# Kernel tuning notes

Measured on AMD Instinct MI355X. Metric: run time of the kernel, lower is better.

## Reference

```python
import jax, jax.numpy as jnp
import numpy as np

MAX_ABS = 1.0          # assumed get_max_abs('T')
DT = 0.01              # forward default dt
TWO_PI = 2.0 * np.pi
B, D, N = 4096, 2048, 4096


def setup_inputs() -> dict:
    key = jax.random.key(0)
    k0, k1 = jax.random.split(key, 2)
    x = jax.random.normal(k0, (B, D), dtype=jnp.float32)
    # nn.Linear params
    W = jax.random.normal(k1, (N, D), dtype=jnp.float32) * (1.0 / np.sqrt(D))
    b = jnp.zeros((N,), dtype=jnp.float32)
    # oscillator params (as initialized in __init__)
    amplitude = jnp.ones((N,), dtype=jnp.float32)
    frequency = jnp.ones((N,), dtype=jnp.float32)
    phase_offset = jnp.zeros((N,), dtype=jnp.float32)
    damping = jnp.full((N,), 0.01, dtype=jnp.float32)
    return {"x": x, "W": W, "b": b, "amplitude": amplitude,
            "frequency": frequency, "phase_offset": phase_offset,
            "damping": damping}


def reference(x, W, b, amplitude, frequency, phase_offset, damping):
    # driving force: [B, N]
    force = x @ W.T + b
    omega_sq = (TWO_PI * frequency) ** 2  # [N]
    # t starts at 0 and is incremented ONCE per forward call
    t = DT

    def step(carry, f):
        state, vel = carry
        accel = -omega_sq * state - damping * vel + f
        vel = vel + accel * DT
        state = state + vel * DT
        return (state, vel), state

    init = (jnp.zeros((N,), x.dtype), jnp.zeros((N,), x.dtype))
    (_, _), states = jax.lax.scan(step, init, force)  # states: [B, N]

    # sinusoid term is identical for every batch step (t fixed within forward)
    osc = amplitude * jnp.sin(TWO_PI * frequency * t + phase_offset)  # [N]
    out = jnp.clip(states + osc, -MAX_ABS, MAX_ABS)
    return out
```

## Files before the change

kernel.cpp:

```cpp
#include <hip/hip_runtime.h>
#include <hip/hip_bf16.h>
#include <math.h>

#define MDIM 4096
#define KDIM 2048
#define NDIM 4096
#define DT   0.01f
#define TWO_PI_F 6.283185307179586f
#define CH 64
#define CL 64
#define TILES (KDIM / 64)

typedef __attribute__((ext_vector_type(8))) short bf16x8;
typedef __attribute__((ext_vector_type(4))) float f32x4;

__device__ __forceinline__ unsigned short f2bf(float f) {
  unsigned int u = __float_as_uint(f);
  u += 0x7FFFu + ((u >> 16) & 1u);
  return (unsigned short)(u >> 16);
}
__device__ __forceinline__ float bf2f(unsigned short u) {
  return __uint_as_float(((unsigned int)u) << 16);
}

__global__ void cast2_bf16_kernel(const float* __restrict__ s0,
                                  unsigned short* __restrict__ d0,
                                  const float* __restrict__ s1,
                                  unsigned short* __restrict__ d1,
                                  int n4each) {
  int i = blockIdx.x * blockDim.x + threadIdx.x;
  const float4* sp;
  ushort4* dp;
  int j;
  if (i < n4each) { sp = (const float4*)s0; dp = (ushort4*)d0; j = i; }
  else            { sp = (const float4*)s1; dp = (ushort4*)d1; j = i - n4each; }
  float4 v = sp[j];
  ushort4 o;
  o.x = f2bf(v.x); o.y = f2bf(v.y); o.z = f2bf(v.z); o.w = f2bf(v.w);
  dp[j] = o;
}


__device__ __forceinline__ void gload16(const unsigned short* g,
                                        unsigned short* l) {
  __builtin_amdgcn_global_load_lds(
      (const __attribute__((address_space(1))) unsigned int*)g,
      (__attribute__((address_space(3))) unsigned int*)l, 16, 0, 0);
}

#define WAITVM(n) asm volatile("s_waitcnt vmcnt(" #n ")" ::: "memory")
#define WAITLGKM(n) asm volatile("s_waitcnt lgkmcnt(" #n ")" ::: "memory")
#define SCHEDB() __builtin_amdgcn_sched_barrier(0)

__global__ __launch_bounds__(512, 2) void gemm_scan256_kernel(
    const unsigned short* __restrict__ A,
    const unsigned short* __restrict__ Bm,
    const float* __restrict__ bias,
    const float* __restrict__ freq,
    const float* __restrict__ damp,
    unsigned short* __restrict__ zpart,
    float* __restrict__ chunkS,
    float* __restrict__ chunkV) {
  extern __shared__ __align__(16) unsigned short smem[];

  const int tid  = threadIdx.x;
  const int lane = tid & 63;
  const int w    = tid >> 6;
  const int wr   = w >> 2;
  const int wc   = w & 3;
  const int q    = lane >> 4;
  const int lm   = lane & 15;

  const int bid = blockIdx.x;
  const int wg  = (bid & 7) * 32 + (bid >> 3);
  const int tm  = wg >> 4;
  const int tn  = wg & 15;
  const int bM  = tm * 256;
  const int bN  = tn * 256;

  const int srow  = w * 16 + (lane >> 2);
  const int sslot = (lane & 3) ^ ((lane >> 3) & 3);
  const unsigned short* gA = A  + (size_t)(bM + srow) * KDIM + sslot * 8;
  const unsigned short* gB = Bm + (size_t)(bN + srow) * KDIM + sslot * 8;
  const int ldst = w * 512 + lane * 8;

#define SUNIT(mat, u, ks, rh)                                              \
  gload16((mat ? gB : gA) + (size_t)(rh) * 128 * KDIM + (u) * 64 + (ks) * 32, \
          smem + ((u) & 1) * 32768 + (mat) * 16384 + (ks) * 8192 +         \
              (rh) * 4096 + ldst)

  const int flane = (lm >> 1) & 3;
  const int aoff  = (wr * 128 + lm) * 32 + ((q ^ flane) * 8);
  const int boff  = 16384 + (wc * 64 + lm) * 32 + ((q ^ flane) * 8);

  f32x4 acc[8][4];
#pragma unroll
  for (int i = 0; i < 8; i++)
#pragma unroll
    for (int j = 0; j < 4; j++) acc[i][j] = (f32x4){0.f, 0.f, 0.f, 0.f};

  SUNIT(1, 0, 0, 0); SUNIT(1, 0, 0, 1);
  SUNIT(0, 0, 0, 0); SUNIT(0, 0, 0, 1);
  SUNIT(1, 0, 1, 0); SUNIT(1, 0, 1, 1);
  SUNIT(0, 0, 1, 0); SUNIT(0, 0, 1, 1);
  SUNIT(1, 1, 0, 0); SUNIT(1, 1, 0, 1);
  SUNIT(0, 1, 0, 0); SUNIT(0, 1, 0, 1);
  SUNIT(1, 1, 1, 0); SUNIT(1, 1, 1, 1);

#define LDA4(dst, BUFO, KS, MH)                                            \
  _Pragma("unroll") for (int m = 0; m < 4; ++m) dst[m] =                   \
      *(const bf16x8*)&smem[(BUFO) + (KS) + (MH) + aoff + m * 512]
#define LDB4(dst, BUFO, KS)                                                \
  _Pragma("unroll") for (int n = 0; n < 4; ++n) dst[n] =                   \
      *(const bf16x8*)&smem[(BUFO) + (KS) + boff + n * 512]
#define MFMA16(AF, BF, MB)                                                 \
  __builtin_amdgcn_s_setprio(1);                                          \
  _Pragma("unroll") for (int m = 0; m < 4; ++m)                            \
      _Pragma("unroll") for (int n = 0; n < 4; ++n)                        \
          acc[(MB) + m][n] = __builtin_amdgcn_mfma_f32_16x16x32_bf16(      \
              AF[m], BF[n], acc[(MB) + m][n], 0, 0, 0);                    \
  __builtin_amdgcn_s_setprio(0)

  bf16x8 af[4], bfr[4];

  WAITVM(10);
  __builtin_amdgcn_s_barrier();
  LDA4(af, 0, 0, 0);
  LDB4(bfr, 0, 0);
  SCHEDB();

#pragma unroll 2
  for (int t = 0; t < TILES; ++t) {
    const int bufo  = (t & 1) * 32768;
    const int nbufo = ((t + 1) & 1) * 32768;

    __builtin_amdgcn_s_barrier();
    if (t + 1 < TILES) { SUNIT(0, t + 1, 1, 0); SUNIT(0, t + 1, 1, 1); }
    WAITLGKM(0); SCHEDB();
    MFMA16(af, bfr, 0);
    LDA4(af, bufo, 0, 2048);
    SCHEDB();

    if (t < TILES - 1) { WAITVM(8); } else { WAITVM(0); }
    __builtin_amdgcn_s_barrier();
    if (t + 2 < TILES) { SUNIT(1, t + 2, 0, 0); SUNIT(1, t + 2, 0, 1); }
    WAITLGKM(0); SCHEDB();
    MFMA16(af, bfr, 4);
    LDA4(af, bufo, 8192, 0);
    LDB4(bfr, bufo, 8192);
    SCHEDB();

    __builtin_amdgcn_s_barrier();
    if (t + 2 < TILES) { SUNIT(0, t + 2, 0, 0); SUNIT(0, t + 2, 0, 1); }
    WAITLGKM(0); SCHEDB();
    MFMA16(af, bfr, 0);
    LDA4(af, bufo, 8192, 2048);
    SCHEDB();

    if (t < TILES - 2) { WAITVM(8); }
    else if (t == TILES - 2) { WAITVM(4); }
    __builtin_amdgcn_s_barrier();
    if (t + 2 < TILES) { SUNIT(1, t + 2, 1, 0); SUNIT(1, t + 2, 1, 1); }
    WAITLGKM(0); SCHEDB();
    MFMA16(af, bfr, 4);
    if (t + 1 < TILES) {
      LDA4(af, nbufo, 0, 0);
      LDB4(bfr, nbufo, 0);
      SCHEDB();
    }
  }
#undef LDA4
#undef LDB4
#undef MFMA16
#undef SUNIT

  __syncthreads();

#pragma unroll
  for (int n = 0; n < 4; ++n) {
    const float bz = bias[bN + wc * 64 + n * 16 + lm];
#pragma unroll
    for (int M = 0; M < 8; ++M)
#pragma unroll
      for (int rr = 0; rr < 4; ++rr) {
        const int row = wr * 128 + M * 16 + q * 4 + rr;
        const int col = wc * 64 + ((n ^ q) * 16) + lm;
        smem[row * 256 + col] = f2bf(acc[M][n][rr] + bz);
      }
  }
  __syncthreads();

  {
    const int col  = tid & 255;
    const int ch0  = (tid >> 8) * 2;
    const int gcol = bN + col;
    const float om  = TWO_PI_F * freq[gcol];
    const float osq = om * om;
    const float dp  = damp[gcol];
#pragma unroll
    for (int cc = 0; cc < 2; ++cc) {
      const int ch = ch0 + cc;
      float s = 0.f, v = 0.f;
#pragma unroll 8
      for (int i = 0; i < CL; ++i) {
        const int row = ch * 64 + i;
        const int idx = row * 256 + (col ^ (((i >> 2) & 3) << 4));
        float f = bf2f(smem[idx]);
        v += (-osq * s - dp * v + f) * DT;
        s += v * DT;
        smem[idx] = f2bf(s);
      }
      const int chunk = tm * 4 + ch;
      chunkS[chunk * NDIM + gcol] = s;
      chunkV[chunk * NDIM + gcol] = v;
    }
  }
  __syncthreads();

#pragma unroll
  for (int k = 0; k < 16; ++k) {
    const int slot = tid + 512 * k;
    const int row  = slot >> 5;
    const int grp  = slot & 31;
    const int sgrp = grp ^ (((row >> 2) & 3) << 1);
    *(uint4*)&zpart[(size_t)(bM + row) * NDIM + bN + grp * 8] =
        *(const uint4*)&smem[row * 256 + sgrp * 8];
  }
}

__global__ void scan_pass2_inplace(float* __restrict__ chunkS,
                                   float* __restrict__ chunkV,
                                   const float* __restrict__ freq,
                                   const float* __restrict__ damp) {
  int n = blockIdx.x * blockDim.x + threadIdx.x;
  float om = TWO_PI_F * freq[n];
  float osq = om * om;
  float dp = damp[n];
  float a00 = 1.f - osq * DT * DT, a01 = DT * (1.f - dp * DT);
  float a10 = -osq * DT,           a11 = 1.f - dp * DT;
#pragma unroll
  for (int i = 0; i < 6; i++) {
    float b00 = a00 * a00 + a01 * a10;
    float b01 = a00 * a01 + a01 * a11;
    float b10 = a10 * a00 + a11 * a10;
    float b11 = a10 * a01 + a11 * a11;
    a00 = b00; a01 = b01; a10 = b10; a11 = b11;
  }
  float cs = 0.f, cv = 0.f;
#pragma unroll 8
  for (int c = 0; c < CH; c++) {
    float ls = chunkS[c * NDIM + n];
    float lv = chunkV[c * NDIM + n];
    chunkS[c * NDIM + n] = cs;
    chunkV[c * NDIM + n] = cv;
    float ns = a00 * cs + a01 * cv + ls;
    float nv = a10 * cs + a11 * cv + lv;
    cs = ns; cv = nv;
  }
}

__global__ void scan_out_carry4(const unsigned short* __restrict__ zpart,
                                const float* __restrict__ amp,
                                const float* __restrict__ freq,
                                const float* __restrict__ phase,
                                const float* __restrict__ damp,
                                const float* __restrict__ carryS,
                                const float* __restrict__ carryV,
                                float* __restrict__ out) {
  int gid = blockIdx.x * blockDim.x + threadIdx.x;
  int n4 = gid & (NDIM / 4 - 1);
  int cq = gid >> 10;
  int c  = cq >> 2;
  int qq = cq & 3;
  int n  = n4 * 4;

  float4 fr = *(const float4*)&freq[n];
  float4 dv = *(const float4*)&damp[n];
  float4 am = *(const float4*)&amp[n];
  float4 ph = *(const float4*)&phase[n];
  float omv[4] = {TWO_PI_F * fr.x, TWO_PI_F * fr.y, TWO_PI_F * fr.z, TWO_PI_F * fr.w};
  float dpv[4] = {dv.x, dv.y, dv.z, dv.w};
  float amv[4] = {am.x, am.y, am.z, am.w};
  float phv[4] = {ph.x, ph.y, ph.z, ph.w};
  float m00[4], m01[4], m10[4], m11[4], osc[4];
#pragma unroll
  for (int j = 0; j < 4; j++) {
    float osq = omv[j] * omv[j];
    m00[j] = 1.f - osq * DT * DT;  m01[j] = DT * (1.f - dpv[j] * DT);
    m10[j] = -osq * DT;            m11[j] = 1.f - dpv[j] * DT;
    osc[j] = amv[j] * sinf(omv[j] * DT + phv[j]);
  }

  float4 csv = *(const float4*)&carryS[c * NDIM + n];
  float4 cvv = *(const float4*)&carryV[c * NDIM + n];
  float cs[4] = {csv.x, csv.y, csv.z, csv.w};
  float cv[4] = {cvv.x, cvv.y, cvv.z, cvv.w};
  float hs[4], hv[4];
#pragma unroll
  for (int j = 0; j < 4; j++) {
    float p00 = m00[j], p01 = m01[j], p10 = m10[j], p11 = m11[j];
#pragma unroll
    for (int k = 0; k < 4; k++) {
      float b00 = p00 * p00 + p01 * p10;
      float b01 = p00 * p01 + p01 * p11;
      float b10 = p10 * p00 + p11 * p10;
      float b11 = p10 * p01 + p11 * p11;
      p00 = b00; p01 = b01; p10 = b10; p11 = b11;
    }
    float j00 = 1.f, j01 = 0.f, j10 = 0.f, j11 = 1.f;
    for (int k = 0; k < qq; k++) {
      float b00 = j00 * p00 + j01 * p10;
      float b01 = j00 * p01 + j01 * p11;
      float b10 = j10 * p00 + j11 * p10;
      float b11 = j10 * p01 + j11 * p11;
      j00 = b00; j01 = b01; j10 = b10; j11 = b11;
    }
    hs[j] = j00 * cs[j] + j01 * cv[j];
    hv[j] = j10 * cs[j] + j11 * cv[j];
  }

  const size_t r0 = (size_t)c * CL + qq * 16;
  const unsigned short* zp = zpart + r0 * NDIM + n;
  float* op = out + r0 * NDIM + n;
#pragma unroll 4
  for (int i = 0; i < 16; ++i) {
    ushort4 zv = *(const ushort4*)&zp[(size_t)i * NDIM];
    float z[4] = {bf2f(zv.x), bf2f(zv.y), bf2f(zv.z), bf2f(zv.w)};
    float o[4];
#pragma unroll
    for (int j = 0; j < 4; j++) {
      float t = m00[j] * hs[j] + m01[j] * hv[j];
      float u = m10[j] * hs[j] + m11[j] * hv[j];
      hs[j] = t; hv[j] = u;
      o[j] = fminf(1.f, fmaxf(-1.f, hs[j] + z[j] + osc[j]));
    }
    *(float4*)&op[(size_t)i * NDIM] = (float4){o[0], o[1], o[2], o[3]};
  }
}

__global__ __launch_bounds__(256, 2) void gemm_bt_kernel(
    const unsigned short* __restrict__ A,
    const unsigned short* __restrict__ Bm,
    const float* __restrict__ bias,
    unsigned short* __restrict__ C) {
  __shared__ __align__(16) unsigned short sA[128 * 32];
  __shared__ __align__(16) unsigned short sB[128 * 32];

  const int tid  = threadIdx.x;
  const int lane = tid & 63;
  const int wave = tid >> 6;
  const int wr = wave >> 1;
  const int wc = wave & 1;
  const int q  = lane >> 4;
  const int lm = lane & 15;

  const int bM = blockIdx.x * 128;
  const int bN = blockIdx.y * 128;

  f32x4 acc[4][4];
#pragma unroll
  for (int i = 0; i < 4; i++)
#pragma unroll
    for (int j = 0; j < 4; j++) acc[i][j] = (f32x4){0.f, 0.f, 0.f, 0.f};

  const int idx0 = tid;
  const int idx1 = tid + 256;
  const int r0 = idx0 >> 2, g0 = idx0 & 3;
  const int r1 = idx1 >> 2, g1 = idx1 & 3;
  const int dst0 = r0 * 32 + ((g0 ^ ((r0 >> 1) & 3)) * 8);
  const int dst1 = r1 * 32 + ((g1 ^ ((r1 >> 1) & 3)) * 8);
  const unsigned short* gA0 = A  + (size_t)(bM + r0) * KDIM + g0 * 8;
  const unsigned short* gA1 = A  + (size_t)(bM + r1) * KDIM + g1 * 8;
  const unsigned short* gB0 = Bm + (size_t)(bN + r0) * KDIM + g0 * 8;
  const unsigned short* gB1 = Bm + (size_t)(bN + r1) * KDIM + g1 * 8;
  const int rq = (q ^ ((lm >> 1) & 3)) * 8;

  for (int k0 = 0; k0 < KDIM; k0 += 32) {
    uint4 av0 = *(const uint4*)(gA0 + k0);
    uint4 av1 = *(const uint4*)(gA1 + k0);
    uint4 bv0 = *(const uint4*)(gB0 + k0);
    uint4 bv1 = *(const uint4*)(gB1 + k0);
    __syncthreads();
    *(uint4*)&sA[dst0] = av0;
    *(uint4*)&sA[dst1] = av1;
    *(uint4*)&sB[dst0] = bv0;
    *(uint4*)&sB[dst1] = bv1;
    __syncthreads();

    bf16x8 af[4], bfr[4];
#pragma unroll
    for (int mt = 0; mt < 4; mt++)
      af[mt]  = *(const bf16x8*)&sA[(wr * 64 + mt * 16 + lm) * 32 + rq];
#pragma unroll
    for (int nt = 0; nt < 4; nt++)
      bfr[nt] = *(const bf16x8*)&sB[(wc * 64 + nt * 16 + lm) * 32 + rq];

#pragma unroll
    for (int mt = 0; mt < 4; mt++)
#pragma unroll
      for (int nt = 0; nt < 4; nt++)
        acc[mt][nt] = __builtin_amdgcn_mfma_f32_16x16x32_bf16(
            af[mt], bfr[nt], acc[mt][nt], 0, 0, 0);
  }

#pragma unroll
  for (int nt = 0; nt < 4; nt++) {
    const int col = bN + wc * 64 + nt * 16 + lm;
    const float bz = bias[col];
#pragma unroll
    for (int mt = 0; mt < 4; mt++) {
      const int row0 = bM + wr * 64 + mt * 16 + q * 4;
#pragma unroll
      for (int r = 0; r < 4; r++)
        C[(size_t)(row0 + r) * NDIM + col] = f2bf(acc[mt][nt][r] + bz);
    }
  }
}

__global__ void scan_pass1(const unsigned short* __restrict__ force,
                           const float* __restrict__ freq,
                           const float* __restrict__ damp,
                           float* __restrict__ chunkS,
                           float* __restrict__ chunkV) {
  int gid = blockIdx.x * blockDim.x + threadIdx.x;
  int n4 = gid & (NDIM / 4 - 1);
  int c  = gid >> 10;
  int n  = n4 * 4;
  float4 fr = *(const float4*)&freq[n];
  float4 dv = *(const float4*)&damp[n];
  float osq[4] = {TWO_PI_F * fr.x, TWO_PI_F * fr.y, TWO_PI_F * fr.z, TWO_PI_F * fr.w};
  float dp[4]  = {dv.x, dv.y, dv.z, dv.w};
  float s[4] = {0.f, 0.f, 0.f, 0.f}, v[4] = {0.f, 0.f, 0.f, 0.f};
#pragma unroll
  for (int j = 0; j < 4; j++) osq[j] *= osq[j];
  const unsigned short* fp = force + (size_t)c * CL * NDIM + n;
#pragma unroll 4
  for (int i = 0; i < CL; i++) {
    ushort4 fv = *(const ushort4*)&fp[(size_t)i * NDIM];
    float f[4] = {bf2f(fv.x), bf2f(fv.y), bf2f(fv.z), bf2f(fv.w)};
#pragma unroll
    for (int j = 0; j < 4; j++) {
      float a = -osq[j] * s[j] - dp[j] * v[j] + f[j];
      v[j] += a * DT;
      s[j] += v[j] * DT;
    }
  }
  *(float4*)&chunkS[c * NDIM + n] = (float4){s[0], s[1], s[2], s[3]};
  *(float4*)&chunkV[c * NDIM + n] = (float4){v[0], v[1], v[2], v[3]};
}

__global__ void scan_pass2(const float* __restrict__ chunkS,
                           const float* __restrict__ chunkV,
                           const float* __restrict__ freq,
                           const float* __restrict__ damp,
                           float* __restrict__ carryS,
                           float* __restrict__ carryV) {
  int n = blockIdx.x * blockDim.x + threadIdx.x;
  float om = TWO_PI_F * freq[n];
  float osq = om * om;
  float dp = damp[n];
  float a00 = 1.f - osq * DT * DT, a01 = DT * (1.f - dp * DT);
  float a10 = -osq * DT,           a11 = 1.f - dp * DT;
#pragma unroll
  for (int i = 0; i < 6; i++) {
    float b00 = a00 * a00 + a01 * a10;
    float b01 = a00 * a01 + a01 * a11;
    float b10 = a10 * a00 + a11 * a10;
    float b11 = a10 * a01 + a11 * a11;
    a00 = b00; a01 = b01; a10 = b10; a11 = b11;
  }
  float cs = 0.f, cv = 0.f;
#pragma unroll 8
  for (int c = 0; c < CH; c++) {
    carryS[c * NDIM + n] = cs;
    carryV[c * NDIM + n] = cv;
    float ls = chunkS[c * NDIM + n];
    float lv = chunkV[c * NDIM + n];
    float ns = a00 * cs + a01 * cv + ls;
    float nv = a10 * cs + a11 * cv + lv;
    cs = ns; cv = nv;
  }
}

__global__ void scan_pass3(const unsigned short* __restrict__ force,
                           const float* __restrict__ amp,
                           const float* __restrict__ freq,
                           const float* __restrict__ phase,
                           const float* __restrict__ damp,
                           const float* __restrict__ carryS,
                           const float* __restrict__ carryV,
                           float* __restrict__ out) {
  int gid = blockIdx.x * blockDim.x + threadIdx.x;
  int n4 = gid & (NDIM / 4 - 1);
  int c  = gid >> 10;
  int n  = n4 * 4;
  float4 fr = *(const float4*)&freq[n];
  float4 dv = *(const float4*)&damp[n];
  float4 am = *(const float4*)&amp[n];
  float4 ph = *(const float4*)&phase[n];
  float om[4] = {TWO_PI_F * fr.x, TWO_PI_F * fr.y, TWO_PI_F * fr.z, TWO_PI_F * fr.w};
  float dp[4] = {dv.x, dv.y, dv.z, dv.w};
  float osq[4], osc[4], s[4], v[4];
  float amv[4] = {am.x, am.y, am.z, am.w};
  float phv[4] = {ph.x, ph.y, ph.z, ph.w};
#pragma unroll
  for (int j = 0; j < 4; j++) {
    osq[j] = om[j] * om[j];
    osc[j] = amv[j] * sinf(om[j] * DT + phv[j]);
  }
  float4 csv = *(const float4*)&carryS[c * NDIM + n];
  float4 cvv = *(const float4*)&carryV[c * NDIM + n];
  s[0] = csv.x; s[1] = csv.y; s[2] = csv.z; s[3] = csv.w;
  v[0] = cvv.x; v[1] = cvv.y; v[2] = cvv.z; v[3] = cvv.w;
  const unsigned short* fp = force + (size_t)c * CL * NDIM + n;
  float* op = out + (size_t)c * CL * NDIM + n;
#pragma unroll 4
  for (int i = 0; i < CL; i++) {
    ushort4 fv = *(const ushort4*)&fp[(size_t)i * NDIM];
    float f[4] = {bf2f(fv.x), bf2f(fv.y), bf2f(fv.z), bf2f(fv.w)};
    float o[4];
#pragma unroll
    for (int j = 0; j < 4; j++) {
      float a = -osq[j] * s[j] - dp[j] * v[j] + f[j];
      v[j] += a * DT;
      s[j] += v[j] * DT;
      o[j] = fminf(1.f, fmaxf(-1.f, s[j] + osc[j]));
    }
    *(float4*)&op[(size_t)i * NDIM] = (float4){o[0], o[1], o[2], o[3]};
  }
}

extern "C" void kernel_launch(void* const* d_in, const int* in_sizes, int n_in,
                              void* d_out, int out_size, void* d_ws, size_t ws_size,
                              hipStream_t stream) {
  const float* x     = (const float*)d_in[0];
  const float* W     = (const float*)d_in[1];
  const float* bias  = (const float*)d_in[2];
  const float* amp   = (const float*)d_in[3];
  const float* freq  = (const float*)d_in[4];
  const float* phase = (const float*)d_in[5];
  const float* damp  = (const float*)d_in[6];

  const size_t MiB = 1024 * 1024;
  const int n4each = MDIM * KDIM / 4;

  if (ws_size >= 66 * MiB) {
    unsigned short* xbf   = (unsigned short*)d_ws;
    unsigned short* wbf   = xbf + (size_t)MDIM * KDIM;
    unsigned short* zpart = wbf + (size_t)NDIM * KDIM;
    float* chunkS = (float*)((char*)d_ws + 64 * MiB);
    float* chunkV = chunkS + CH * NDIM;

    static bool attr_done = false;
    if (!attr_done) {
      (void)hipFuncSetAttribute((const void*)gemm_scan256_kernel,
                                hipFuncAttributeMaxDynamicSharedMemorySize,
                                131072);
      attr_done = true;
    }

    cast2_bf16_kernel<<<(2 * n4each + 255) / 256, 256, 0, stream>>>(
        x, xbf, W, wbf, n4each);
    gemm_scan256_kernel<<<dim3(256), dim3(512), 131072, stream>>>(
        xbf, wbf, bias, freq, damp, zpart, chunkS, chunkV);
    scan_pass2_inplace<<<NDIM / 256, 256, 0, stream>>>(chunkS, chunkV,
                                                       freq, damp);
    scan_out_carry4<<<CH * 4 * NDIM / 4 / 256, 256, 0, stream>>>(
        zpart, amp, freq, phase, damp, chunkS, chunkV, (float*)d_out);
  } else {
    dim3 gg(MDIM / 128, NDIM / 128);
    unsigned short* xbf   = (unsigned short*)d_ws;
    unsigned short* wbf   = xbf + (size_t)MDIM * KDIM;
    unsigned short* force = wbf + (size_t)NDIM * KDIM;
    float* chunkS = (float*)d_ws;
    float* chunkV = chunkS + CH * NDIM;
    float* carryS = chunkV + CH * NDIM;
    float* carryV = carryS + CH * NDIM;

    cast2_bf16_kernel<<<(2 * n4each + 255) / 256, 256, 0, stream>>>(
        x, xbf, W, wbf, n4each);
    gemm_bt_kernel<<<gg, 256, 0, stream>>>(xbf, wbf, bias, force);
    scan_pass1<<<CH * NDIM / 4 / 256, 256, 0, stream>>>(force, freq, damp,
                                                        chunkS, chunkV);
    scan_pass2<<<NDIM / 256, 256, 0, stream>>>(chunkS, chunkV, freq, damp,
                                               carryS, carryV);
    scan_pass3<<<CH * NDIM / 4 / 256, 256, 0, stream>>>(
        force, amp, freq, phase, damp, carryS, carryV, (float*)d_out);
  }
}
```

Baseline: 205.1 us.

## Fuse chunk-carry scan and output pass into GEMM via cooperative grid sync

Merges the GEMM+local-scan kernel, the chunk-carry pass and the output pass into one cooperative kernel that keeps the locally scanned tile in LDS. After a grid-wide sync, each block recomputes its own carry-in by serially folding the preceding chunk summaries. It then writes the clamped output straight from LDS. This drops the bf16 zpart round trip through global memory and two kernel launches. The cost is a grid barrier, a redundant per-block carry recomputation of up to 64 chunks, and the need for all 256 blocks to be co-resident.

```diff
diff --git a/kernel.cpp b/kernel.cpp
--- a/kernel.cpp
+++ b/kernel.cpp
@@ -1,6 +1,9 @@
 #include <hip/hip_runtime.h>
 #include <hip/hip_bf16.h>
+#include <hip/hip_cooperative_groups.h>
 #include <math.h>
+
+namespace cg = cooperative_groups;
 
 #define MDIM 4096
 #define KDIM 2048
@@ -52,15 +55,17 @@
 #define WAITLGKM(n) asm volatile("s_waitcnt lgkmcnt(" #n ")" ::: "memory")
 #define SCHEDB() __builtin_amdgcn_sched_barrier(0)
 
-__global__ __launch_bounds__(512, 2) void gemm_scan256_kernel(
+__global__ __launch_bounds__(512, 2) void gemm_scan_out_kernel(
     const unsigned short* __restrict__ A,
     const unsigned short* __restrict__ Bm,
     const float* __restrict__ bias,
     const float* __restrict__ freq,
     const float* __restrict__ damp,
-    unsigned short* __restrict__ zpart,
+    const float* __restrict__ amp,
+    const float* __restrict__ phase,
     float* __restrict__ chunkS,
-    float* __restrict__ chunkV) {
+    float* __restrict__ chunkV,
+    float* __restrict__ out) {
   extern __shared__ __align__(16) unsigned short smem[];
 
   const int tid  = threadIdx.x;
@@ -215,126 +220,68 @@
       chunkV[chunk * NDIM + gcol] = v;
     }
   }
-  __syncthreads();
-
-#pragma unroll
-  for (int k = 0; k < 16; ++k) {
-    const int slot = tid + 512 * k;
-    const int row  = slot >> 5;
-    const int grp  = slot & 31;
-    const int sgrp = grp ^ (((row >> 2) & 3) << 1);
-    *(uint4*)&zpart[(size_t)(bM + row) * NDIM + bN + grp * 8] =
-        *(const uint4*)&smem[row * 256 + sgrp * 8];
-  }
-}
-
-__global__ void scan_pass2_inplace(float* __restrict__ chunkS,
-                                   float* __restrict__ chunkV,
-                                   const float* __restrict__ freq,
-                                   const float* __restrict__ damp) {
-  int n = blockIdx.x * blockDim.x + threadIdx.x;
-  float om = TWO_PI_F * freq[n];
-  float osq = om * om;
-  float dp = damp[n];
-  float a00 = 1.f - osq * DT * DT, a01 = DT * (1.f - dp * DT);
-  float a10 = -osq * DT,           a11 = 1.f - dp * DT;
-#pragma unroll
-  for (int i = 0; i < 6; i++) {
-    float b00 = a00 * a00 + a01 * a10;
-    float b01 = a00 * a01 + a01 * a11;
-    float b10 = a10 * a00 + a11 * a10;
-    float b11 = a10 * a01 + a11 * a11;
-    a00 = b00; a01 = b01; a10 = b10; a11 = b11;
-  }
-  float cs = 0.f, cv = 0.f;
-#pragma unroll 8
-  for (int c = 0; c < CH; c++) {
-    float ls = chunkS[c * NDIM + n];
-    float lv = chunkV[c * NDIM + n];
-    chunkS[c * NDIM + n] = cs;
-    chunkV[c * NDIM + n] = cv;
-    float ns = a00 * cs + a01 * cv + ls;
-    float nv = a10 * cs + a11 * cv + lv;
-    cs = ns; cv = nv;
-  }
-}
-
-__global__ void scan_out_carry4(const unsigned short* __restrict__ zpart,
-                                const float* __restrict__ amp,
-                                const float* __restrict__ freq,
-                                const float* __restrict__ phase,
-                                const float* __restrict__ damp,
-                                const float* __restrict__ carryS,
-                                const float* __restrict__ carryV,
-                                float* __restrict__ out) {
-  int gid = blockIdx.x * blockDim.x + threadIdx.x;
-  int n4 = gid & (NDIM / 4 - 1);
-  int cq = gid >> 10;
-  int c  = cq >> 2;
-  int qq = cq & 3;
-  int n  = n4 * 4;
-
-  float4 fr = *(const float4*)&freq[n];
-  float4 dv = *(const float4*)&damp[n];
-  float4 am = *(const float4*)&amp[n];
-  float4 ph = *(const float4*)&phase[n];
-  float omv[4] = {TWO_PI_F * fr.x, TWO_PI_F * fr.y, TWO_PI_F * fr.z, TWO_PI_F * fr.w};
-  float dpv[4] = {dv.x, dv.y, dv.z, dv.w};
-  float amv[4] = {am.x, am.y, am.z, am.w};
-  float phv[4] = {ph.x, ph.y, ph.z, ph.w};
-  float m00[4], m01[4], m10[4], m11[4], osc[4];
-#pragma unroll
-  for (int j = 0; j < 4; j++) {
-    float osq = omv[j] * omv[j];
-    m00[j] = 1.f - osq * DT * DT;  m01[j] = DT * (1.f - dpv[j] * DT);
-    m10[j] = -osq * DT;            m11[j] = 1.f - dpv[j] * DT;
-    osc[j] = amv[j] * sinf(omv[j] * DT + phv[j]);
-  }
-
-  float4 csv = *(const float4*)&carryS[c * NDIM + n];
-  float4 cvv = *(const float4*)&carryV[c * NDIM + n];
-  float cs[4] = {csv.x, csv.y, csv.z, csv.w};
-  float cv[4] = {cvv.x, cvv.y, cvv.z, cvv.w};
-  float hs[4], hv[4];
-#pragma unroll
-  for (int j = 0; j < 4; j++) {
-    float p00 = m00[j], p01 = m01[j], p10 = m10[j], p11 = m11[j];
-#pragma unroll
-    for (int k = 0; k < 4; k++) {
-      float b00 = p00 * p00 + p01 * p10;
-      float b01 = p00 * p01 + p01 * p11;
-      float b10 = p10 * p00 + p11 * p10;
-      float b11 = p10 * p01 + p11 * p11;
-      p00 = b00; p01 = b01; p10 = b10; p11 = b11;
-    }
-    float j00 = 1.f, j01 = 0.f, j10 = 0.f, j11 = 1.f;
-    for (int k = 0; k < qq; k++) {
-      float b00 = j00 * p00 + j01 * p10;
-      float b01 = j00 * p01 + j01 * p11;
-      float b10 = j10 * p00 + j11 * p10;
-      float b11 = j10 * p01 + j11 * p11;
-      j00 = b00; j01 = b01; j10 = b10; j11 = b11;
-    }
-    hs[j] = j00 * cs[j] + j01 * cv[j];
-    hv[j] = j10 * cs[j] + j11 * cv[j];
-  }
-
-  const size_t r0 = (size_t)c * CL + qq * 16;
-  const unsigned short* zp = zpart + r0 * NDIM + n;
-  float* op = out + r0 * NDIM + n;
+
+  cg::this_grid().sync();
+
+  const int cp   = tid & 127;
+  const int hh   = tid >> 7;
+  const int col0 = cp * 2;
+  const int gc   = bN + col0;
+
+  float2 fr2 = *(const float2*)&freq[gc];
+  float2 dm2 = *(const float2*)&damp[gc];
+  float2 am2 = *(const float2*)&amp[gc];
+  float2 ph2 = *(const float2*)&phase[gc];
+  const float omA = TWO_PI_F * fr2.x, omB = TWO_PI_F * fr2.y;
+  const float oqA = omA * omA,        oqB = omB * omB;
+  const float mA00 = 1.f - oqA * DT * DT, mA01 = DT * (1.f - dm2.x * DT);
+  const float mA10 = -oqA * DT,           mA11 = 1.f - dm2.x * DT;
+  const float mB00 = 1.f - oqB * DT * DT, mB01 = DT * (1.f - dm2.y * DT);
+  const float mB10 = -oqB * DT,           mB11 = 1.f - dm2.y * DT;
+  const float oscA = am2.x * sinf(omA * DT + ph2.x);
+  const float oscB = am2.y * sinf(omB * DT + ph2.y);
+
+  float aA00 = mA00, aA01 = mA01, aA10 = mA10, aA11 = mA11;
+  float aB00 = mB00, aB01 = mB01, aB10 = mB10, aB11 = mB11;
+#pragma unroll
+  for (int i = 0; i < 6; ++i) {
+    float b00, b01, b10, b11;
+    b00 = aA00*aA00 + aA01*aA10; b01 = aA00*aA01 + aA01*aA11;
+    b10 = aA10*aA00 + aA11*aA10; b11 = aA10*aA01 + aA11*aA11;
+    aA00 = b00; aA01 = b01; aA10 = b10; aA11 = b11;
+    b00 = aB00*aB00 + aB01*aB10; b01 = aB00*aB01 + aB01*aB11;
+    b10 = aB10*aB00 + aB11*aB10; b11 = aB10*aB01 + aB11*aB11;
+    aB00 = b00; aB01 = b01; aB10 = b10; aB11 = b11;
+  }
+
+  float csA = 0.f, cvA = 0.f, csB = 0.f, cvB = 0.f;
+  const int cEnd = tm * 4 + hh;
 #pragma unroll 4
-  for (int i = 0; i < 16; ++i) {
-    ushort4 zv = *(const ushort4*)&zp[(size_t)i * NDIM];
-    float z[4] = {bf2f(zv.x), bf2f(zv.y), bf2f(zv.z), bf2f(zv.w)};
-    float o[4];
-#pragma unroll
-    for (int j = 0; j < 4; j++) {
-      float t = m00[j] * hs[j] + m01[j] * hv[j];
-      float u = m10[j] * hs[j] + m11[j] * hv[j];
-      hs[j] = t; hv[j] = u;
-      o[j] = fminf(1.f, fmaxf(-1.f, hs[j] + z[j] + osc[j]));
-    }
-    *(float4*)&op[(size_t)i * NDIM] = (float4){o[0], o[1], o[2], o[3]};
+  for (int c = 0; c < cEnd; ++c) {
+    float2 ls = *(const float2*)&chunkS[c * NDIM + gc];
+    float2 lv = *(const float2*)&chunkV[c * NDIM + gc];
+    float nsA = aA00*csA + aA01*cvA + ls.x;
+    float nvA = aA10*csA + aA11*cvA + lv.x;
+    float nsB = aB00*csB + aB01*cvB + ls.y;
+    float nvB = aB10*csB + aB11*cvB + lv.y;
+    csA = nsA; cvA = nvA; csB = nsB; cvB = nvB;
+  }
+
+  float* op = out + (size_t)(bM + hh * 64) * NDIM + gc;
+#pragma unroll 4
+  for (int i = 0; i < 64; ++i) {
+    const int row = hh * 64 + i;
+    const unsigned int zz = *(const unsigned int*)
+        &smem[row * 256 + (col0 ^ (((i >> 2) & 3) << 4))];
+    const float zA = bf2f((unsigned short)(zz & 0xffffu));
+    const float zB = bf2f((unsigned short)(zz >> 16));
+    float tA = mA00*csA + mA01*cvA, uA = mA10*csA + mA11*cvA;
+    float tB = mB00*csB + mB01*cvB, uB = mB10*csB + mB11*cvB;
+    csA = tA; cvA = uA; csB = tB; cvB = uB;
+    float2 o2;
+    o2.x = fminf(1.f, fmaxf(-1.f, csA + zA + oscA));
+    o2.y = fminf(1.f, fmaxf(-1.f, csB + zB + oscB));
+    *(float2*)&op[(size_t)i * NDIM] = o2;
   }
 }
 
@@ -544,16 +491,16 @@
   const size_t MiB = 1024 * 1024;
   const int n4each = MDIM * KDIM / 4;
 
-  if (ws_size >= 66 * MiB) {
-    unsigned short* xbf   = (unsigned short*)d_ws;
-    unsigned short* wbf   = xbf + (size_t)MDIM * KDIM;
-    unsigned short* zpart = wbf + (size_t)NDIM * KDIM;
-    float* chunkS = (float*)((char*)d_ws + 64 * MiB);
+  if (ws_size >= 36 * MiB) {
+    unsigned short* xbf = (unsigned short*)d_ws;
+    unsigned short* wbf = xbf + (size_t)MDIM * KDIM;
+    float* chunkS = (float*)((char*)d_ws + 32 * MiB);
     float* chunkV = chunkS + CH * NDIM;
+    float* outf   = (float*)d_out;
 
     static bool attr_done = false;
     if (!attr_done) {
-      (void)hipFuncSetAttribute((const void*)gemm_scan256_kernel,
+      (void)hipFuncSetAttribute((const void*)gemm_scan_out_kernel,
                                 hipFuncAttributeMaxDynamicSharedMemorySize,
                                 131072);
       attr_done = true;
@@ -561,12 +508,16 @@
 
     cast2_bf16_kernel<<<(2 * n4each + 255) / 256, 256, 0, stream>>>(
         x, xbf, W, wbf, n4each);
-    gemm_scan256_kernel<<<dim3(256), dim3(512), 131072, stream>>>(
-        xbf, wbf, bias, freq, damp, zpart, chunkS, chunkV);
-    scan_pass2_inplace<<<NDIM / 256, 256, 0, stream>>>(chunkS, chunkV,
-                                                       freq, damp);
-    scan_out_carry4<<<CH * 4 * NDIM / 4 / 256, 256, 0, stream>>>(
-        zpart, amp, freq, phase, damp, chunkS, chunkV, (float*)d_out);
+
+    const unsigned short* a_ = xbf;
+    const unsigned short* b_ = wbf;
+    void* kargs[] = {(void*)&a_,    (void*)&b_,    (void*)&bias,
+                     (void*)&freq,  (void*)&damp,  (void*)&amp,
+                     (void*)&phase, (void*)&chunkS, (void*)&chunkV,
+                     (void*)&outf};
+    (void)hipLaunchCooperativeKernel((const void*)gemm_scan_out_kernel,
+                                     dim3(256), dim3(512), kargs,
+                                     131072, stream);
   } else {
     dim3 gg(MDIM / 128, NDIM / 128);
     unsigned short* xbf   = (unsigned short*)d_ws;
```

Result: slower. 242.7 us (+18.3%).
